# Kernel optimization log

Hardware: AMD Instinct MI355X
Metric: run time of the kernel (lower is better)

The kernel has to match this reference:

```python
import jax, jax.numpy as jnp
import numpy as np

N_NODES = 50000
N_EDGES = 800000
D = 128


def setup_inputs() -> dict:
    key = jax.random.key(0)
    ks = jax.random.split(key, 8)
    h = jax.random.normal(ks[0], (N_NODES, D), dtype=jnp.float32)
    src = jax.random.randint(ks[1], (N_EDGES,), 0, N_NODES, dtype=jnp.int64)
    dst = jax.random.randint(ks[2], (N_EDGES,), 0, N_NODES, dtype=jnp.int64)
    # Glorot-ish init for the three GraphConv weights
    scale = 1.0 / np.sqrt(D)
    W0 = jax.random.normal(ks[3], (D, D), dtype=jnp.float32) * scale
    W1 = jax.random.normal(ks[4], (D, D), dtype=jnp.float32) * scale
    W2 = jax.random.normal(ks[5], (D, D), dtype=jnp.float32) * scale
    b0 = jnp.zeros((D,), dtype=jnp.float32)
    b1 = jnp.zeros((D,), dtype=jnp.float32)
    b2 = jnp.zeros((D,), dtype=jnp.float32)
    return {"h": h, "src": src, "dst": dst, "W0": W0, "b0": b0,
            "W1": W1, "b1": b1, "W2": W2, "b2": b2}


def _graph_conv(x, src, dst, W, b, n_nodes):
    """DGL GraphConv, norm='both', activation=ReLU.
    in_feats == out_feats -> aggregate first, then matmul W."""
    ones = jnp.ones_like(src, dtype=x.dtype)
    out_deg = jnp.clip(jax.ops.segment_sum(ones, src, num_segments=n_nodes), 1.0)
    in_deg = jnp.clip(jax.ops.segment_sum(ones, dst, num_segments=n_nodes), 1.0)
    x = x * (out_deg ** -0.5)[:, None]          # src-side normalization
    m = jax.ops.segment_sum(x[src], dst, num_segments=n_nodes)  # sparse aggregation
    m = m * (in_deg ** -0.5)[:, None]           # dst-side normalization
    return jax.nn.relu(m @ W + b)


def reference(h, src, dst, W0, b0, W1, b1, W2, b2):
    n = h.shape[0]
    h = _graph_conv(h, src, dst, W0, b0, n)
    h = _graph_conv(h, src, dst, W1, b1, n)
    h = _graph_conv(h, src, dst, W2, b2, n)
    return h
```

## Files before the change

### kernel.cpp

```cpp
#include <hip/hip_runtime.h>

#define N_NODES 50000
#define N_EDGES 800000
#define D 128
#define CAP 48
#define NPADN 50176

#define PACKB 24

#define ABLK 400
#define AEDGES (N_EDGES / ABLK)
#define DBW 256
#define DNB 196
#define DCAP 6144
#define SBW 512
#define SNB 98
#define BCAP 10240

typedef __attribute__((ext_vector_type(4))) float f32x4;
typedef __attribute__((ext_vector_type(8))) short s16x8;

__device__ inline unsigned short f32_to_bf16_rtne(float f) {
    union { float f; unsigned u; } c; c.f = f;
    unsigned u = c.u;
    u += 0x7FFF + ((u >> 16) & 1);
    return (unsigned short)(u >> 16);
}
__device__ inline float bf16_to_f32(unsigned short h) {
    union { unsigned u; float f; } c; c.u = ((unsigned)h) << 16;
    return c.f;
}
__device__ inline unsigned pack_bf2(float a, float b) {
    return (unsigned)f32_to_bf16_rtne(a) | ((unsigned)f32_to_bf16_rtne(b) << 16);
}
__device__ inline void unpack_bf2(unsigned u, float& a, float& b) {
    union { unsigned u; float f; } c0, c1;
    c0.u = u << 16; c1.u = u & 0xFFFF0000u;
    a = c0.f; b = c1.f;
}
__device__ inline void acc_uint4(uint4 v, float* a) {
    float f0, f1;
    unpack_bf2(v.x, f0, f1); a[0] += f0; a[1] += f1;
    unpack_bf2(v.y, f0, f1); a[2] += f0; a[3] += f1;
    unpack_bf2(v.z, f0, f1); a[4] += f0; a[5] += f1;
    unpack_bf2(v.w, f0, f1); a[6] += f0; a[7] += f1;
}


__global__ __launch_bounds__(256) void build_bin(const int* __restrict__ src,
                                                 const int* __restrict__ dst,
                                                 int* __restrict__ gcurD,
                                                 int* __restrict__ gcurS,
                                                 unsigned long long* __restrict__ dbin,
                                                 unsigned short* __restrict__ sbin,
                                                 const float* __restrict__ W0,
                                                 const float* __restrict__ W1,
                                                 const float* __restrict__ W2,
                                                 s16x8* __restrict__ wpk) {
    int b = blockIdx.x;
    if (b < ABLK) {
        __shared__ int cntD[DNB], baseD[DNB], c2D[DNB];
        __shared__ int cntS[SNB], baseS[SNB], c2S[SNB];
        for (int i = threadIdx.x; i < DNB; i += 256) { cntD[i] = 0; c2D[i] = 0; }
        for (int i = threadIdx.x; i < SNB; i += 256) { cntS[i] = 0; c2S[i] = 0; }
        __syncthreads();
        int e0 = b * AEDGES;
        for (int i = threadIdx.x; i < AEDGES; i += 256) {
            int s = src[e0 + i], d = dst[e0 + i];
            atomicAdd(&cntD[d >> 8], 1);
            atomicAdd(&cntS[s >> 9], 1);
        }
        __syncthreads();
        for (int i = threadIdx.x; i < DNB; i += 256) baseD[i] = atomicAdd(&gcurD[i], cntD[i]);
        for (int i = threadIdx.x; i < SNB; i += 256) baseS[i] = atomicAdd(&gcurS[i], cntS[i]);
        __syncthreads();
        for (int i = threadIdx.x; i < AEDGES; i += 256) {
            int e = e0 + i;
            int s = src[e], d = dst[e];
            int bd = d >> 8;
            int rd = atomicAdd(&c2D[bd], 1);
            int od = baseD[bd] + rd;
            if (od < DCAP)
                dbin[(size_t)bd * DCAP + od] =
                    ((unsigned long long)(unsigned)e << 32) | ((unsigned)(d & 255) << 16) | (unsigned)s;
            int bs = s >> 9;
            int rs = atomicAdd(&c2S[bs], 1);
            int os = baseS[bs] + rs;
            if (os < BCAP) sbin[bs * BCAP + os] = (unsigned short)s;
        }
    } else {
        int wid = (b - ABLK) * 4 + (threadIdx.x >> 6);
        if (wid >= 96) return;
        int lane = threadIdx.x & 63;
        int layer = wid / 32, rem = wid % 32;
        int ct = rem >> 2, ks = rem & 3;
        const float* W = (layer == 0) ? W0 : (layer == 1) ? W1 : W2;
        int col = ct * 16 + (lane & 15);
        int k0  = ks * 32 + (lane >> 4) * 8;
        s16x8 hi, lo;
#pragma unroll
        for (int j = 0; j < 8; j++) {
            float w = W[(k0 + j) * D + col];
            unsigned short h = f32_to_bf16_rtne(w);
            hi[j] = (short)h;
            lo[j] = (short)f32_to_bf16_rtne(w - bf16_to_f32(h));
        }
        int idx = layer * 4096 + (ct * 4 + ks) * 64 + lane;
        wpk[idx]        = hi;
        wpk[idx + 2048] = lo;
    }
}


__global__ __launch_bounds__(256) void fill_sort(const unsigned long long* __restrict__ dbin,
                                                 const int* __restrict__ gcurD,
                                                 unsigned short* __restrict__ slots,
                                                 int* __restrict__ cursor,
                                                 const unsigned short* __restrict__ sbin,
                                                 const int* __restrict__ gcurS,
                                                 int* __restrict__ odeg) {
    __shared__ unsigned key[256 * 49];
    __shared__ unsigned short sv[256 * CAP];
    __shared__ int cur[256];
    __shared__ int scnt[SBW];
    int b = blockIdx.x;
    if (b < DNB) {
        int t = threadIdx.x;
        cur[t] = 0;
        __syncthreads();
        int n = min(gcurD[b], DCAP);
        const unsigned long long* eb = dbin + (size_t)b * DCAP;
        for (int i = t; i < n; i += 256) {
            unsigned long long w = eb[i];
            int dl = (int)((w >> 16) & 255);
            int p = atomicAdd(&cur[dl], 1);
            if (p < CAP) {
                key[dl * 49 + p] = (unsigned)(w >> 32);
                sv[dl * CAP + p] = (unsigned short)(w & 0xFFFFu);
            }
        }
        __syncthreads();
        {
            int m = min(cur[t], CAP);
            int bk = t * 49, bs = t * CAP;
            for (int i = 1; i < m; i++) {
                unsigned ki = key[bk + i];
                unsigned short si = sv[bs + i];
                int j = i - 1;
                while (j >= 0 && key[bk + j] > ki) {
                    key[bk + j + 1] = key[bk + j];
                    sv[bs + j + 1] = sv[bs + j];
                    j--;
                }
                key[bk + j + 1] = ki;
                sv[bs + j + 1] = si;
            }
        }
        __syncthreads();
        int n0 = b * DBW;
        unsigned* dw = (unsigned*)(slots + (size_t)n0 * CAP);
        const unsigned* sw = (const unsigned*)sv;
        for (int i = t; i < DBW * CAP / 2; i += 256) dw[i] = sw[i];
        cursor[n0 + t] = cur[t];
    } else {
        int bb = b - DNB;
        for (int i = threadIdx.x; i < SBW; i += 256) scnt[i] = 0;
        __syncthreads();
        int nE = min(gcurS[bb], BCAP);
        const unsigned short* es = sbin + (size_t)bb * BCAP;
        for (int i = threadIdx.x; i < nE; i += 256)
            atomicAdd(&scnt[es[i] & (SBW - 1)], 1);
        __syncthreads();
        int n0 = bb * SBW;
        for (int i = threadIdx.x; i < SBW; i += 256)
            if (n0 + i < N_NODES) odeg[n0 + i] = scnt[i];
    }
}


__global__ __launch_bounds__(256) void hconv(const float4* __restrict__ h,
                                             const int* __restrict__ odeg,
                                             float* __restrict__ s_out,
                                             uint2* __restrict__ hbA,
                                             uint2* __restrict__ hbB) {
    int gid = blockIdx.x * 256 + threadIdx.x;
    const int total = N_NODES * 32;
    if (gid < total) {
        int node = gid >> 5;
        float so = rsqrtf(fmaxf((float)odeg[node], 1.0f));
        if ((gid & 31) == 0) s_out[node] = so;
        float4 v = h[gid];
        hbA[gid] = make_uint2(pack_bf2(so * v.x, so * v.y), pack_bf2(so * v.z, so * v.w));
    } else if (gid < total + 32) {
        hbA[total + (gid - total)] = make_uint2(0u, 0u);
    } else if (gid < total + 64) {
        hbB[total + (gid - total - 32)] = make_uint2(0u, 0u);
    }
}


__global__ __launch_bounds__(256) void fused_layer(const uint4* __restrict__ x,
                                                   const unsigned short* __restrict__ slots,
                                                   const int* __restrict__ deg,
                                                   const s16x8* __restrict__ wpk,
                                                   const float* __restrict__ bias,
                                                   const float* __restrict__ s_out,
                                                   float* __restrict__ outf,
                                                   unsigned short* __restrict__ outb) {
    __shared__ s16x8 mHI[16 * 17];
    __shared__ s16x8 mLO[16 * 17];
    int tid = threadIdx.x;
    int row0 = blockIdx.x * 16;

    {
        int nloc = tid >> 4;
        int l    = tid & 15;
        int node = row0 + nloc;
        int dgraw = deg[node];
        int dg = min(dgraw, CAP);
        int base = node * CAP;
        int idx0 = (l      < dg) ? (int)slots[base + l]      : N_NODES;
        int idx1 = (16 + l < dg) ? (int)slots[base + 16 + l] : N_NODES;
        int idx2 = (32 + l < dg) ? (int)slots[base + 32 + l] : N_NODES;

        float a[8];
#pragma unroll
        for (int j = 0; j < 8; j++) a[j] = 0.f;

        int nr = (dg + 7) >> 3;
        for (int r = 0; r < nr; r++) {
            int c = r >> 1;
            int v = (c == 0) ? idx0 : ((c == 1) ? idx1 : idx2);
            int k = (r & 1) * 8;
            int s0 = __shfl(v, k + 0, 16), s1 = __shfl(v, k + 1, 16);
            int s2 = __shfl(v, k + 2, 16), s3 = __shfl(v, k + 3, 16);
            int s4 = __shfl(v, k + 4, 16), s5 = __shfl(v, k + 5, 16);
            int s6 = __shfl(v, k + 6, 16), s7 = __shfl(v, k + 7, 16);
            uint4 g0 = x[s0 * 16 + l];
            uint4 g1 = x[s1 * 16 + l];
            uint4 g2 = x[s2 * 16 + l];
            uint4 g3 = x[s3 * 16 + l];
            uint4 g4 = x[s4 * 16 + l];
            uint4 g5 = x[s5 * 16 + l];
            uint4 g6 = x[s6 * 16 + l];
            uint4 g7 = x[s7 * 16 + l];
            acc_uint4(g0, a); acc_uint4(g1, a); acc_uint4(g2, a); acc_uint4(g3, a);
            acc_uint4(g4, a); acc_uint4(g5, a); acc_uint4(g6, a); acc_uint4(g7, a);
        }
        float si = rsqrtf(fmaxf((float)dgraw, 1.0f));
        s16x8 ahi, alo;
#pragma unroll
        for (int j = 0; j < 8; j++) {
            float av = a[j] * si;
            unsigned short hh = f32_to_bf16_rtne(av);
            ahi[j] = (short)hh;
            alo[j] = (short)f32_to_bf16_rtne(av - bf16_to_f32(hh));
        }
        mHI[nloc * 17 + l] = ahi;
        mLO[nloc * 17 + l] = alo;
    }
    __syncthreads();

    int wv = tid >> 6;
    int lane = tid & 63;
    int arow = lane & 15, aq = lane >> 4;
    int ct0 = wv * 2, ct1 = ct0 + 1;
    f32x4 acc0 = (f32x4)0.f, acc1 = (f32x4)0.f;

#pragma unroll
    for (int ks = 0; ks < 4; ks++) {
        s16x8 ahi = mHI[arow * 17 + ks * 4 + aq];
        s16x8 alo = mLO[arow * 17 + ks * 4 + aq];
        int idx0 = (ct0 * 4 + ks) * 64 + lane;
        int idx1 = (ct1 * 4 + ks) * 64 + lane;
        s16x8 b0h = wpk[idx0], b0l = wpk[idx0 + 2048];
        s16x8 b1h = wpk[idx1], b1l = wpk[idx1 + 2048];
        acc0 = __builtin_amdgcn_mfma_f32_16x16x32_bf16(ahi, b0h, acc0, 0, 0, 0);
        acc0 = __builtin_amdgcn_mfma_f32_16x16x32_bf16(alo, b0h, acc0, 0, 0, 0);
        acc0 = __builtin_amdgcn_mfma_f32_16x16x32_bf16(ahi, b0l, acc0, 0, 0, 0);
        acc1 = __builtin_amdgcn_mfma_f32_16x16x32_bf16(ahi, b1h, acc1, 0, 0, 0);
        acc1 = __builtin_amdgcn_mfma_f32_16x16x32_bf16(alo, b1h, acc1, 0, 0, 0);
        acc1 = __builtin_amdgcn_mfma_f32_16x16x32_bf16(ahi, b1l, acc1, 0, 0, 0);
    }

    int crow0 = aq * 4;
    float so4[4];
    if (outb) {
#pragma unroll
        for (int r = 0; r < 4; r++) so4[r] = s_out[row0 + crow0 + r];
    }
    int colA = ct0 * 16 + arow, colB = ct1 * 16 + arow;
    float bA = bias[colA], bB = bias[colB];
#pragma unroll
    for (int r = 0; r < 4; r++) {
        size_t rowoff = (size_t)(row0 + crow0 + r) * D;
        float vA = fmaxf(acc0[r] + bA, 0.f);
        float vB = fmaxf(acc1[r] + bB, 0.f);
        if (outf) { outf[rowoff + colA] = vA; outf[rowoff + colB] = vB; }
        if (outb) {
            outb[rowoff + colA] = f32_to_bf16_rtne(so4[r] * vA);
            outb[rowoff + colB] = f32_to_bf16_rtne(so4[r] * vB);
        }
    }
}


extern "C" void kernel_launch(void* const* d_in, const int* in_sizes, int n_in,
                              void* d_out, int out_size, void* d_ws, size_t ws_size,
                              hipStream_t stream) {
    const float* h  = (const float*)d_in[0];
    const int*  src = (const int*)d_in[1];
    const int*  dst = (const int*)d_in[2];
    const float* W0 = (const float*)d_in[3];
    const float* b0 = (const float*)d_in[4];
    const float* W1 = (const float*)d_in[5];
    const float* b1 = (const float*)d_in[6];
    const float* W2 = (const float*)d_in[7];
    const float* b2 = (const float*)d_in[8];
    float* out = (float*)d_out;

    char* w = (char*)d_ws;
    auto carve = [&](size_t bytes) -> void* {
        void* p = (void*)w;
        w += (bytes + 255) & ~(size_t)255;
        return p;
    };
    int*      gcurD   = (int*)carve((DNB + 128) * sizeof(int));
    int*      gcurS   = gcurD + DNB;
    int*      cursor  = (int*)carve(NPADN * sizeof(int));
    int*      odeg    = (int*)carve(N_NODES * sizeof(int));
    float*    s_out   = (float*)carve(N_NODES * sizeof(float));
    unsigned long long* dbin = (unsigned long long*)carve((size_t)DNB * DCAP * 8);
    unsigned short* slots = (unsigned short*)carve((size_t)NPADN * CAP * sizeof(unsigned short));
    unsigned short* sbin  = (unsigned short*)carve((size_t)SNB * BCAP * sizeof(unsigned short));
    unsigned short* actA  = (unsigned short*)carve((size_t)(N_NODES + 1) * D * 2);
    unsigned short* actB  = (unsigned short*)carve((size_t)(N_NODES + 1) * D * 2);
    s16x8*    wpk     = (s16x8*)carve(3 * 4096 * sizeof(s16x8));

    hipMemsetAsync(gcurD, 0, (DNB + 128) * sizeof(int), stream);
    build_bin<<<ABLK + PACKB, 256, 0, stream>>>(src, dst, gcurD, gcurS, dbin, sbin,
                                                W0, W1, W2, wpk);
    fill_sort<<<DNB + SNB, 256, 0, stream>>>(dbin, gcurD, slots, cursor,
                                             sbin, gcurS, odeg);
    hconv<<<(N_NODES * 32 + 64 + 255) / 256, 256, 0, stream>>>((const float4*)h, odeg, s_out,
                                                               (uint2*)actA, (uint2*)actB);

    const int GRID = N_NODES / 16;

    fused_layer<<<GRID, 256, 0, stream>>>((const uint4*)actA, slots, cursor,
                                          wpk, b0, s_out, nullptr, actB);
    fused_layer<<<GRID, 256, 0, stream>>>((const uint4*)actB, slots, cursor,
                                          wpk + 4096, b1, s_out, nullptr, actA);
    fused_layer<<<GRID, 256, 0, stream>>>((const uint4*)actA, slots, cursor,
                                          wpk + 8192, b2, s_out, out, nullptr);
}
```

Baseline: 264.7 us.

## Split fill_sort buckets in half and use parallel rank sort

Each destination bucket of 256 nodes is now handled by two blocks, each covering 128 nodes, which doubles the block count and reduces LDS per block. The per-node serial insertion sort is replaced by a rank sort in which two threads per node each compute ranks for alternate edges by counting smaller keys, then scatter into a second buffer. This aims to cut the serial sort latency and raise occupancy. The cost is that each block rereads the full bucket input, and O(m^2) comparisons per node. Equal keys would get the same rank and collide.

After: 234.0 us. 1.13x faster.

```diff
diff --git a/kernel.cpp b/kernel.cpp
--- a/kernel.cpp
+++ b/kernel.cpp
@@ -13,6 +13,8 @@
 #define DBW 256
 #define DNB 196
 #define DCAP 6144
+#define FNB (2 * DNB)
+#define HN 128
 #define SBW 512
 #define SNB 98
 #define BCAP 10240
@@ -119,51 +121,55 @@
                                                  const unsigned short* __restrict__ sbin,
                                                  const int* __restrict__ gcurS,
                                                  int* __restrict__ odeg) {
-    __shared__ unsigned key[256 * 49];
-    __shared__ unsigned short sv[256 * CAP];
-    __shared__ int cur[256];
+    __shared__ unsigned key[HN * 49];
+    __shared__ unsigned short sv[HN * 48];
+    __shared__ unsigned short sv2[HN * 50];
+    __shared__ int cur[HN];
     __shared__ int scnt[SBW];
     int b = blockIdx.x;
-    if (b < DNB) {
+    if (b < FNB) {
+        int bucket = b >> 1, half = b & 1;
         int t = threadIdx.x;
-        cur[t] = 0;
-        __syncthreads();
-        int n = min(gcurD[b], DCAP);
-        const unsigned long long* eb = dbin + (size_t)b * DCAP;
+        if (t < HN) cur[t] = 0;
+        __syncthreads();
+        int n = min(gcurD[bucket], DCAP);
+        const unsigned long long* eb = dbin + (size_t)bucket * DCAP;
         for (int i = t; i < n; i += 256) {
             unsigned long long w = eb[i];
             int dl = (int)((w >> 16) & 255);
-            int p = atomicAdd(&cur[dl], 1);
-            if (p < CAP) {
-                key[dl * 49 + p] = (unsigned)(w >> 32);
-                sv[dl * CAP + p] = (unsigned short)(w & 0xFFFFu);
+            if ((dl >> 7) == half) {
+                int d2 = dl & (HN - 1);
+                int p = atomicAdd(&cur[d2], 1);
+                if (p < CAP) {
+                    key[d2 * 49 + p] = (unsigned)(w >> 32);
+                    sv[d2 * 48 + p] = (unsigned short)(w & 0xFFFFu);
+                }
             }
         }
         __syncthreads();
         {
-            int m = min(cur[t], CAP);
-            int bk = t * 49, bs = t * CAP;
-            for (int i = 1; i < m; i++) {
-                unsigned ki = key[bk + i];
-                unsigned short si = sv[bs + i];
-                int j = i - 1;
-                while (j >= 0 && key[bk + j] > ki) {
-                    key[bk + j + 1] = key[bk + j];
-                    sv[bs + j + 1] = sv[bs + j];
-                    j--;
-                }
-                key[bk + j + 1] = ki;
-                sv[bs + j + 1] = si;
+            int node = t & (HN - 1), sub = t >> 7;
+            int m = min(cur[node], CAP);
+            int kb = node * 49, vb = node * 48, ob = node * 50;
+            for (int i = sub; i < m; i += 2) {
+                unsigned ki = key[kb + i];
+                int r = 0;
+#pragma unroll 4
+                for (int j = 0; j < m; j++) r += (key[kb + j] < ki) ? 1 : 0;
+                sv2[ob + r] = sv[vb + i];
             }
         }
         __syncthreads();
-        int n0 = b * DBW;
+        int n0 = bucket * DBW + half * HN;
         unsigned* dw = (unsigned*)(slots + (size_t)n0 * CAP);
-        const unsigned* sw = (const unsigned*)sv;
-        for (int i = t; i < DBW * CAP / 2; i += 256) dw[i] = sw[i];
-        cursor[n0 + t] = cur[t];
+        for (int idx = t; idx < HN * (CAP / 2); idx += 256) {
+            int node = idx / (CAP / 2);
+            int w2 = idx - node * (CAP / 2);
+            dw[idx] = *(const unsigned*)&sv2[node * 50 + w2 * 2];
+        }
+        if (t < HN) cursor[n0 + t] = cur[t];
     } else {
-        int bb = b - DNB;
+        int bb = b - FNB;
         for (int i = threadIdx.x; i < SBW; i += 256) scnt[i] = 0;
         __syncthreads();
         int nE = min(gcurS[bb], BCAP);
@@ -340,7 +346,7 @@
     hipMemsetAsync(gcurD, 0, (DNB + 128) * sizeof(int), stream);
     build_bin<<<ABLK + PACKB, 256, 0, stream>>>(src, dst, gcurD, gcurS, dbin, sbin,
                                                 W0, W1, W2, wpk);
-    fill_sort<<<DNB + SNB, 256, 0, stream>>>(dbin, gcurD, slots, cursor,
+    fill_sort<<<FNB + SNB, 256, 0, stream>>>(dbin, gcurD, slots, cursor,
                                              sbin, gcurS, odeg);
     hconv<<<(N_NODES * 32 + 64 + 255) / 256, 256, 0, stream>>>((const float4*)h, odeg, s_out,
                                                                (uint2*)actA, (uint2*)actB);
```
